# Kernel optimization log

Hardware: AMD Instinct MI355X
Metric: run time of the kernel (lower is better)

## Reference

```python
import jax, jax.numpy as jnp
import numpy as np

BN_EPS = 1e-5


def _bn(x, gamma, beta):
    # BatchNorm1d in training mode: batch mean, biased variance
    m = jnp.mean(x, axis=0)
    v = jnp.var(x, axis=0)
    return (x - m) * jax.lax.rsqrt(v + BN_EPS) * gamma + beta


def _gin_rel(h_src, h_dst, src, dst, W1, W2, g1, b1, g2, b2):
    # GINConv (eps=0): sum-aggregate src features onto dst, add self feature
    n_dst = h_dst.shape[0]
    agg = jax.ops.segment_sum(h_src[src], dst, num_segments=n_dst)  # [N_dst, d]
    x = h_dst + agg
    # MLP: Linear -> BN -> ReLU -> Linear  (both Linears bias=False)
    h = jax.nn.relu(_bn(x @ W1, g1, b1)) @ W2
    # GINBase: BN -> ReLU
    return jax.nn.relu(_bn(h, g2, b2))


def setup_inputs() -> dict:
    key = jax.random.key(0)
    ks = jax.random.split(key, 12)
    N_U, N_I, E, D = 50000, 50000, 640000, 128
    s = 1.0 / np.sqrt(D)
    inp = {
        "h_user": jax.random.normal(ks[0], (N_U, D), jnp.float32),
        "h_item": jax.random.normal(ks[1], (N_I, D), jnp.float32),
        "src_rates": jax.random.randint(ks[2], (E,), 0, N_U, jnp.int32),
        "dst_rates": jax.random.randint(ks[3], (E,), 0, N_I, jnp.int32),
        "src_rev": jax.random.randint(ks[4], (E,), 0, N_I, jnp.int32),
        "dst_rev": jax.random.randint(ks[5], (E,), 0, N_U, jnp.int32),
        "W1_rates": jax.random.normal(ks[6], (D, D), jnp.float32) * s,
        "W2_rates": jax.random.normal(ks[7], (D, D), jnp.float32) * s,
        "g1_rates": jnp.ones((D,), jnp.float32),
        "b1_rates": jnp.zeros((D,), jnp.float32),
        "g2_rates": jnp.ones((D,), jnp.float32),
        "b2_rates": jnp.zeros((D,), jnp.float32),
        "W1_rev": jax.random.normal(ks[8], (D, D), jnp.float32) * s,
        "W2_rev": jax.random.normal(ks[9], (D, D), jnp.float32) * s,
        "g1_rev": jnp.ones((D,), jnp.float32),
        "b1_rev": jnp.zeros((D,), jnp.float32),
        "g2_rev": jnp.ones((D,), jnp.float32),
        "b2_rev": jnp.zeros((D,), jnp.float32),
    }
    return inp


def reference(h_user, h_item, src_rates, dst_rates, src_rev, dst_rev,
              W1_rates, W2_rates, g1_rates, b1_rates, g2_rates, b2_rates,
              W1_rev, W2_rev, g1_rev, b1_rev, g2_rev, b2_rev):
    # relation 'rates': user -> item; relation 'rated_by': item -> user
    out_item = _gin_rel(h_user, h_item, src_rates, dst_rates,
                        W1_rates, W2_rates, g1_rates, b1_rates, g2_rates, b2_rates)
    out_user = _gin_rel(h_item, h_user, src_rev, dst_rev,
                        W1_rev, W2_rev, g1_rev, b1_rev, g2_rev, b2_rev)
    # HeteroGraphConv sums per dst type; one relation per dst type here.
    # GINLayer squeezes each output (no-op for 2D tensors).
    return (out_user, out_item)
```

## Files before the change

### kernel.cpp

```cpp
#include <hip/hip_runtime.h>

#define D 128
static constexpr float BN_EPS = 1e-5f;

typedef __attribute__((ext_vector_type(8))) short short8;
typedef __attribute__((ext_vector_type(4))) float f32x4;

__device__ __forceinline__ unsigned short f2bf(float f)
{
    unsigned u = __builtin_bit_cast(unsigned, f);
    unsigned r = u + 0x7fffu + ((u >> 16) & 1u);
    return (unsigned short)(r >> 16);
}
__device__ __forceinline__ float bflo(unsigned u)
{
    return __builtin_bit_cast(float, u << 16);
}
__device__ __forceinline__ float bfhi(unsigned u)
{
    return __builtin_bit_cast(float, u & 0xffff0000u);
}

struct CsrRel {
    const int* src; const int* dst;
    int* counts; int* offsets; int* bsum; int* perm; int* rank;
    int E; int N; int nscan;
};
struct GatherRel {
    const unsigned short* hb; const float* hdst;
    const int* offsets; const int* perm;
    unsigned short* x; int N;
};
struct GemmRel {
    const unsigned short* X; const unsigned short* Wt;
    const float* insum; const float* insq; const float* gg; const float* bb;
    unsigned short* Y; float* osum; float* osq;
    int N; int ntiles;
};
struct OutRel {
    const unsigned short* z;
    const float* sum; const float* sq; const float* gg; const float* bb;
    float* out; int N;
};

__global__ void convert_h_kernel(const float* __restrict__ hu,
                                 const float* __restrict__ hi,
                                 unsigned short* __restrict__ bu,
                                 unsigned short* __restrict__ bi8,
                                 int nu8, int ni8)
{
    int i = blockIdx.x * blockDim.x + threadIdx.x;
    if (i >= nu8 + ni8) return;
    const float* s; unsigned short* d; int o;
    if (i < nu8) { s = hu; d = bu; o = i; }
    else         { s = hi; d = bi8; o = i - nu8; }
    float4 v0 = reinterpret_cast<const float4*>(s)[o * 2];
    float4 v1 = reinterpret_cast<const float4*>(s)[o * 2 + 1];
    uint4 r;
    r.x = (unsigned)f2bf(v0.x) | ((unsigned)f2bf(v0.y) << 16);
    r.y = (unsigned)f2bf(v0.z) | ((unsigned)f2bf(v0.w) << 16);
    r.z = (unsigned)f2bf(v1.x) | ((unsigned)f2bf(v1.y) << 16);
    r.w = (unsigned)f2bf(v1.z) | ((unsigned)f2bf(v1.w) << 16);
    reinterpret_cast<uint4*>(d)[o] = r;
}

__global__ __launch_bounds__(256) void prep_w_kernel(
    const float* __restrict__ Wa, const float* __restrict__ Wb,
    const float* __restrict__ Wc, const float* __restrict__ Wd,
    unsigned short* __restrict__ wt)
{
    const int wsel = blockIdx.x >> 4;
    const float* W = wsel == 0 ? Wa : wsel == 1 ? Wb : wsel == 2 ? Wc : Wd;
    unsigned short* out = wt + (size_t)wsel * D * D;
    const int tile = blockIdx.x & 15;
    const int k0 = (tile >> 2) * 32, n0 = (tile & 3) * 32;
    __shared__ float s[32][33];
    const int t = threadIdx.x;
    const int r = t >> 3, c = (t & 7) * 4;
    float4 v = *reinterpret_cast<const float4*>(W + (size_t)(k0 + r) * D + n0 + c);
    s[r][c] = v.x; s[r][c + 1] = v.y; s[r][c + 2] = v.z; s[r][c + 3] = v.w;
    __syncthreads();
    unsigned lo = (unsigned)f2bf(s[c][r]) | ((unsigned)f2bf(s[c + 1][r]) << 16);
    unsigned hi = (unsigned)f2bf(s[c + 2][r]) | ((unsigned)f2bf(s[c + 3][r]) << 16);
    *reinterpret_cast<uint2*>(out + (size_t)(n0 + r) * D + k0 + c) =
        make_uint2(lo, hi);
}

__global__ void hist_kernel(CsrRel r0, CsrRel r1)
{
    CsrRel r = blockIdx.y ? r1 : r0;
    int e = blockIdx.x * blockDim.x + threadIdx.x;
    if (e < r.E) r.rank[e] = atomicAdd(&r.counts[r.dst[e]], 1);
}

__global__ __launch_bounds__(256) void scan_partial_kernel(CsrRel rr0, CsrRel rr1)
{
    CsrRel r = blockIdx.y ? rr1 : rr0;
    if ((int)blockIdx.x >= r.nscan) return;
    __shared__ int red[256];
    const int t = threadIdx.x;
    const int base = blockIdx.x * 1024 + t * 4;
    int s = 0;
    if (base + 3 < r.N) {
        int4 q = *reinterpret_cast<const int4*>(r.counts + base);
        s = q.x + q.y + q.z + q.w;
    } else {
        for (int j = 0; j < 4; ++j)
            if (base + j < r.N) s += r.counts[base + j];
    }
    red[t] = s;
    __syncthreads();
    for (int off = 128; off > 0; off >>= 1) {
        if (t < off) red[t] += red[t + off];
        __syncthreads();
    }
    if (t == 0) r.bsum[blockIdx.x] = red[0];
}

__global__ __launch_bounds__(256) void scan_partials_kernel(CsrRel rr0, CsrRel rr1)
{
    CsrRel r = blockIdx.y ? rr1 : rr0;
    __shared__ int part[256];
    const int t = threadIdx.x;
    int v = (t < r.nscan) ? r.bsum[t] : 0;
    part[t] = v;
    __syncthreads();
    for (int off = 1; off < 256; off <<= 1) {
        int tmp = (t >= off) ? part[t - off] : 0;
        __syncthreads();
        part[t] += tmp;
        __syncthreads();
    }
    if (t < r.nscan) r.bsum[t] = part[t] - v;
}

__global__ __launch_bounds__(256) void scan_block_kernel(CsrRel rr0, CsrRel rr1)
{
    CsrRel r = blockIdx.y ? rr1 : rr0;
    if ((int)blockIdx.x >= r.nscan) return;
    __shared__ int part[256];
    const int b = blockIdx.x, t = threadIdx.x;
    const int base = b * 1024 + t * 4;
    int v[4] = {0, 0, 0, 0};
    if (base + 3 < r.N) {
        int4 q = *reinterpret_cast<const int4*>(r.counts + base);
        v[0] = q.x; v[1] = q.y; v[2] = q.z; v[3] = q.w;
    } else {
        for (int j = 0; j < 4; ++j)
            if (base + j < r.N) v[j] = r.counts[base + j];
    }
    int s = v[0] + v[1] + v[2] + v[3];
    part[t] = s;
    __syncthreads();
    for (int off = 1; off < 256; off <<= 1) {
        int tmp = (t >= off) ? part[t - off] : 0;
        __syncthreads();
        part[t] += tmp;
        __syncthreads();
    }
    int excl = part[t] - s + r.bsum[b];
    int o0 = excl, o1 = o0 + v[0], o2 = o1 + v[1], o3 = o2 + v[2];
    if (base + 3 < r.N) {
        *reinterpret_cast<int4*>(r.offsets + base) = make_int4(o0, o1, o2, o3);
    } else {
        int oo[4] = {o0, o1, o2, o3};
        for (int j = 0; j < 4; ++j)
            if (base + j < r.N) r.offsets[base + j] = oo[j];
    }
    if (b == r.nscan - 1 && t == 255) r.offsets[r.N] = r.bsum[b] + part[255];
}

#define FILL_EPT 8
__global__ __launch_bounds__(256) void fill_kernel(CsrRel rr0, CsrRel rr1)
{
    CsrRel r = blockIdx.y ? rr1 : rr0;
    const int bucket = blockIdx.x & 7;
    const int chunk = blockIdx.x >> 3;
    const int nper = (r.N + 7) >> 3;
    const int lo = bucket * nper, hi = lo + nper;
    const int base = chunk * (256 * FILL_EPT) + threadIdx.x;
#pragma unroll
    for (int k = 0; k < FILL_EPT; ++k) {
        int e = base + k * 256;
        if (e < r.E) {
            int d = r.dst[e];
            if (d >= lo && d < hi)
                r.perm[r.offsets[d] + r.rank[e]] = r.src[e];
        }
    }
}

__global__ __launch_bounds__(256) void gather_agg_kernel(GatherRel g0, GatherRel g1)
{
    GatherRel g = blockIdx.y ? g1 : g0;
    int row = blockIdx.x * 4 + (threadIdx.x >> 6);
    row = __builtin_amdgcn_readfirstlane(row);
    if (row >= g.N) return;
    const int c = (threadIdx.x & 63) * 2;
    const int beg = g.offsets[row], end = g.offsets[row + 1];
    float2 acc = *reinterpret_cast<const float2*>(g.hdst + (size_t)row * D + c);
    const unsigned short* hb = g.hb;
    int i = beg;
    for (; i + 3 < end; i += 4) {
        int s0 = g.perm[i], s1 = g.perm[i + 1];
        int s2 = g.perm[i + 2], s3 = g.perm[i + 3];
        unsigned u0 = *reinterpret_cast<const unsigned*>(hb + (size_t)s0 * D + c);
        unsigned u1 = *reinterpret_cast<const unsigned*>(hb + (size_t)s1 * D + c);
        unsigned u2 = *reinterpret_cast<const unsigned*>(hb + (size_t)s2 * D + c);
        unsigned u3 = *reinterpret_cast<const unsigned*>(hb + (size_t)s3 * D + c);
        acc.x += (bflo(u0) + bflo(u1)) + (bflo(u2) + bflo(u3));
        acc.y += (bfhi(u0) + bfhi(u1)) + (bfhi(u2) + bfhi(u3));
    }
    for (; i < end; ++i) {
        unsigned u = *reinterpret_cast<const unsigned*>(hb + (size_t)g.perm[i] * D + c);
        acc.x += bflo(u);
        acc.y += bfhi(u);
    }
    unsigned o = (unsigned)f2bf(acc.x) | ((unsigned)f2bf(acc.y) << 16);
    *reinterpret_cast<unsigned*>(g.x + (size_t)row * D + c) = o;
}

__device__ __forceinline__ unsigned bnpack(unsigned u, float sLo, float sHi,
                                           float bLo, float bHi)
{
    float lo = fmaxf(fmaf(bflo(u), sLo, bLo), 0.f);
    float hi = fmaxf(fmaf(bfhi(u), sHi, bHi), 0.f);
    return (unsigned)f2bf(lo) | ((unsigned)f2bf(hi) << 16);
}

template <bool BN_IN>
__global__ __launch_bounds__(256, 2) void gemm_stats_kernel(GemmRel q0, GemmRel q1)
{
    GemmRel q = blockIdx.y ? q1 : q0;
    const int t = threadIdx.x;
    const int w = t >> 6;
    const int l = t & 63;
    const int lr = l & 15;
    const int lk = (l >> 4) << 3;

    __shared__ float s_sc[D], s_bi[D];
    if constexpr (BN_IN) {
        if (t < D) {
            float inv_n = 1.f / (float)q.N;
            float mean = q.insum[t] * inv_n;
            float var = fmaxf(q.insq[t] * inv_n - mean * mean, 0.f);
            float s = q.gg[t] * rsqrtf(var + BN_EPS);
            s_sc[t] = s;
            s_bi[t] = q.bb[t] - mean * s;
        }
        __syncthreads();
    }

    uint4 wf[4][8];
#pragma unroll
    for (int kk = 0; kk < 4; ++kk)
#pragma unroll
        for (int n = 0; n < 8; ++n)
            wf[kk][n] = *reinterpret_cast<const uint4*>(
                q.Wt + (size_t)(n * 16 + lr) * D + kk * 32 + lk);

    float ps[8], pq[8];
#pragma unroll
    for (int n = 0; n < 8; ++n) { ps[n] = 0.f; pq[n] = 0.f; }

    for (int tile = blockIdx.x; tile < q.ntiles; tile += gridDim.x) {
        const int arow = tile * 64 + w * 16 + lr;
        f32x4 acc[8];
#pragma unroll
        for (int n = 0; n < 8; ++n) acc[n] = (f32x4){0.f, 0.f, 0.f, 0.f};

#pragma unroll
        for (int kk = 0; kk < 4; ++kk) {
            uint4 a4 = make_uint4(0u, 0u, 0u, 0u);
            if (arow < q.N) {
                a4 = *reinterpret_cast<const uint4*>(
                    q.X + (size_t)arow * D + kk * 32 + lk);
                if constexpr (BN_IN) {
                    const int kb = kk * 32 + lk;
                    float4 s0 = *reinterpret_cast<const float4*>(&s_sc[kb]);
                    float4 s1 = *reinterpret_cast<const float4*>(&s_sc[kb + 4]);
                    float4 b0 = *reinterpret_cast<const float4*>(&s_bi[kb]);
                    float4 b1 = *reinterpret_cast<const float4*>(&s_bi[kb + 4]);
                    a4.x = bnpack(a4.x, s0.x, s0.y, b0.x, b0.y);
                    a4.y = bnpack(a4.y, s0.z, s0.w, b0.z, b0.w);
                    a4.z = bnpack(a4.z, s1.x, s1.y, b1.x, b1.y);
                    a4.w = bnpack(a4.w, s1.z, s1.w, b1.z, b1.w);
                }
            }
            short8 a = __builtin_bit_cast(short8, a4);
#pragma unroll
            for (int n = 0; n < 8; ++n)
                acc[n] = __builtin_amdgcn_mfma_f32_16x16x32_bf16(
                    a, __builtin_bit_cast(short8, wf[kk][n]), acc[n], 0, 0, 0);
        }

        const int orow = tile * 64 + w * 16 + (l >> 4) * 4;
#pragma unroll
        for (int n = 0; n < 8; ++n) {
#pragma unroll
            for (int j = 0; j < 4; ++j) {
                float v = acc[n][j];
                ps[n] += v;
                pq[n] += v * v;
                if (orow + j < q.N)
                    q.Y[(size_t)(orow + j) * D + n * 16 + lr] = f2bf(v);
            }
        }
    }

#pragma unroll
    for (int n = 0; n < 8; ++n) {
        ps[n] += __shfl_xor(ps[n], 16); ps[n] += __shfl_xor(ps[n], 32);
        pq[n] += __shfl_xor(pq[n], 16); pq[n] += __shfl_xor(pq[n], 32);
    }
    __shared__ float ssum[4][D], ssq[4][D];
    if (l < 16) {
#pragma unroll
        for (int n = 0; n < 8; ++n) {
            ssum[w][n * 16 + l] = ps[n];
            ssq[w][n * 16 + l]  = pq[n];
        }
    }
    __syncthreads();
    if (t < D) {
        float a = ssum[0][t] + ssum[1][t] + ssum[2][t] + ssum[3][t];
        float b = ssq[0][t] + ssq[1][t] + ssq[2][t] + ssq[3][t];
        atomicAdd(&q.osum[t], a);
        atomicAdd(&q.osq[t], b);
    }
}

__global__ __launch_bounds__(256) void bn_relu_out_kernel(OutRel o0, OutRel o1)
{
    OutRel o = blockIdx.y ? o1 : o0;
    __shared__ float s_sc[D], s_bi[D];
    if (threadIdx.x < D) {
        int c = threadIdx.x;
        float inv_n = 1.f / (float)o.N;
        float mean = o.sum[c] * inv_n;
        float var = fmaxf(o.sq[c] * inv_n - mean * mean, 0.f);
        float s = o.gg[c] * rsqrtf(var + BN_EPS);
        s_sc[c] = s;
        s_bi[c] = o.bb[c] - mean * s;
    }
    __syncthreads();

    const int n8 = o.N * (D / 8);
    for (int i = blockIdx.x * blockDim.x + threadIdx.x; i < n8;
         i += gridDim.x * blockDim.x) {
        uint4 z = reinterpret_cast<const uint4*>(o.z)[i];
        int c = (i * 8) & (D - 1);
        float4 s0 = *reinterpret_cast<const float4*>(&s_sc[c]);
        float4 s1 = *reinterpret_cast<const float4*>(&s_sc[c + 4]);
        float4 b0 = *reinterpret_cast<const float4*>(&s_bi[c]);
        float4 b1 = *reinterpret_cast<const float4*>(&s_bi[c + 4]);
        float4 r0, r1;
        r0.x = fmaxf(fmaf(bflo(z.x), s0.x, b0.x), 0.f);
        r0.y = fmaxf(fmaf(bfhi(z.x), s0.y, b0.y), 0.f);
        r0.z = fmaxf(fmaf(bflo(z.y), s0.z, b0.z), 0.f);
        r0.w = fmaxf(fmaf(bfhi(z.y), s0.w, b0.w), 0.f);
        r1.x = fmaxf(fmaf(bflo(z.z), s1.x, b1.x), 0.f);
        r1.y = fmaxf(fmaf(bfhi(z.z), s1.y, b1.y), 0.f);
        r1.z = fmaxf(fmaf(bflo(z.w), s1.z, b1.z), 0.f);
        r1.w = fmaxf(fmaf(bfhi(z.w), s1.w, b1.w), 0.f);
        reinterpret_cast<float4*>(o.out)[i * 2] = r0;
        reinterpret_cast<float4*>(o.out)[i * 2 + 1] = r1;
    }
}

extern "C" void kernel_launch(void* const* d_in, const int* in_sizes, int n_in,
                              void* d_out, int out_size, void* d_ws, size_t ws_size,
                              hipStream_t stream)
{
    const float* h_user   = (const float*)d_in[0];
    const float* h_item   = (const float*)d_in[1];
    const int* src_rates  = (const int*)d_in[2];
    const int* dst_rates  = (const int*)d_in[3];
    const int* src_rev    = (const int*)d_in[4];
    const int* dst_rev    = (const int*)d_in[5];
    const float* W1_rates = (const float*)d_in[6];
    const float* W2_rates = (const float*)d_in[7];
    const float* g1_rates = (const float*)d_in[8];
    const float* b1_rates = (const float*)d_in[9];
    const float* g2_rates = (const float*)d_in[10];
    const float* b2_rates = (const float*)d_in[11];
    const float* W1_rev   = (const float*)d_in[12];
    const float* W2_rev   = (const float*)d_in[13];
    const float* g1_rev   = (const float*)d_in[14];
    const float* b1_rev   = (const float*)d_in[15];
    const float* g2_rev   = (const float*)d_in[16];
    const float* b2_rev   = (const float*)d_in[17];

    const int n_user = in_sizes[0] / D;
    const int n_item = in_sizes[1] / D;
    const int E1 = in_sizes[2];
    const int E2 = in_sizes[4];

    char* p = (char*)d_ws;
    auto alloc = [&](size_t bytes) {
        char* q = p;
        p += (bytes + 255) & ~(size_t)255;
        return q;
    };
    unsigned short* hbu = (unsigned short*)alloc((size_t)n_user * D * 2);
    unsigned short* hbi = (unsigned short*)alloc((size_t)n_item * D * 2);
    unsigned short* xz0 = (unsigned short*)alloc((size_t)n_item * D * 2);
    unsigned short* xz1 = (unsigned short*)alloc((size_t)n_user * D * 2);
    unsigned short* yb0 = (unsigned short*)alloc((size_t)n_item * D * 2);
    unsigned short* yb1 = (unsigned short*)alloc((size_t)n_user * D * 2);
    unsigned short* wt  = (unsigned short*)alloc((size_t)4 * D * D * 2);
    char* zbeg = p;
    float* stats   = (float*)alloc((size_t)8 * D * 4);
    int* counts0   = (int*)alloc((size_t)n_item * 4);
    int* counts1   = (int*)alloc((size_t)n_user * 4);
    size_t zbytes  = (size_t)(p - zbeg);
    int* offsets0  = (int*)alloc(((size_t)n_item + 1) * 4);
    int* offsets1  = (int*)alloc(((size_t)n_user + 1) * 4);
    int* bsum0     = (int*)alloc((size_t)256 * 4);
    int* bsum1     = (int*)alloc((size_t)256 * 4);
    int* perm0     = (int*)alloc((size_t)E1 * 4);
    int* perm1     = (int*)alloc((size_t)E2 * 4);
    int* rank0     = (int*)alloc((size_t)E1 * 4);
    int* rank1     = (int*)alloc((size_t)E2 * 4);

    float* out_user = (float*)d_out;
    float* out_item = out_user + (size_t)n_user * D;

    const int nu8 = n_user * D / 8, ni8 = n_item * D / 8;
    convert_h_kernel<<<(nu8 + ni8 + 255) / 256, 256, 0, stream>>>(
        h_user, h_item, hbu, hbi, nu8, ni8);
    prep_w_kernel<<<64, 256, 0, stream>>>(W1_rates, W2_rates, W1_rev, W2_rev, wt);
    hipMemsetAsync(zbeg, 0, zbytes, stream);

    float* st0 = stats;
    float* st1 = stats + 4 * D;

    CsrRel c0 = {src_rates, dst_rates, counts0, offsets0, bsum0, perm0, rank0,
                 E1, n_item, (n_item + 1023) / 1024};
    CsrRel c1 = {src_rev, dst_rev, counts1, offsets1, bsum1, perm1, rank1,
                 E2, n_user, (n_user + 1023) / 1024};

    int emax = E1 > E2 ? E1 : E2;
    int eb = (emax + 255) / 256;
    int ns = c0.nscan > c1.nscan ? c0.nscan : c1.nscan;
    hist_kernel<<<dim3(eb, 2), 256, 0, stream>>>(c0, c1);
    scan_partial_kernel<<<dim3(ns, 2), 256, 0, stream>>>(c0, c1);
    scan_partials_kernel<<<dim3(1, 2), 256, 0, stream>>>(c0, c1);
    scan_block_kernel<<<dim3(ns, 2), 256, 0, stream>>>(c0, c1);
    int fb = 8 * ((emax + 256 * FILL_EPT - 1) / (256 * FILL_EPT));
    fill_kernel<<<dim3(fb, 2), 256, 0, stream>>>(c0, c1);

    GatherRel ga0 = {hbu, h_item, offsets0, perm0, xz0, n_item};
    GatherRel ga1 = {hbi, h_user, offsets1, perm1, xz1, n_user};
    int ab = ((n_item > n_user ? n_item : n_user) + 3) / 4;
    gather_agg_kernel<<<dim3(ab, 2), 256, 0, stream>>>(ga0, ga1);

    const int nt0 = (n_item + 63) / 64, nt1 = (n_user + 63) / 64;
    int gx = nt0 > nt1 ? nt0 : nt1;
    if (gx > 256) gx = 256;

    GemmRel q10 = {xz0, wt,             nullptr, nullptr, nullptr, nullptr,
                   yb0, st0, st0 + D, n_item, nt0};
    GemmRel q11 = {xz1, wt + 2 * D * D, nullptr, nullptr, nullptr, nullptr,
                   yb1, st1, st1 + D, n_user, nt1};
    gemm_stats_kernel<false><<<dim3(gx, 2), 256, 0, stream>>>(q10, q11);

    GemmRel q20 = {yb0, wt + D * D,     st0, st0 + D, g1_rates, b1_rates,
                   xz0, st0 + 2 * D, st0 + 3 * D, n_item, nt0};
    GemmRel q21 = {yb1, wt + 3 * D * D, st1, st1 + D, g1_rev, b1_rev,
                   xz1, st1 + 2 * D, st1 + 3 * D, n_user, nt1};
    gemm_stats_kernel<true><<<dim3(gx, 2), 256, 0, stream>>>(q20, q21);

    OutRel o0 = {xz0, st0 + 2 * D, st0 + 3 * D, g2_rates, b2_rates,
                 out_item, n_item};
    OutRel o1 = {xz1, st1 + 2 * D, st1 + 3 * D, g2_rev, b2_rev,
                 out_user, n_user};
    int n8m = (n_item > n_user ? n_item : n_user) * (D / 8);
    int ob = (n8m + 255) / 256;
    if (ob > 2048) ob = 2048;
    bn_relu_out_kernel<<<dim3(ob, 2), 256, 0, stream>>>(o0, o1);
}
```

Before: 223.7 us.

## Build CSR histogram with LDS-privatized per-bucket-chunk counters instead of global atomics

Replaces global atomic histogramming with blocks that each own a destination bucket and edge chunk and count into shared memory. A new per-destination prefix pass over chunks produces the per-chunk offsets and the total counts, and the fill kernel adds the chunk offset to the local rank. This removes contended global atomics and the memset of the counts array. In exchange it adds a kernel launch and a partial-count buffer, and each block rescans its whole edge chunk, so every edge is read once per bucket. The 8192-entry shared array must hold a full bucket width, which caps N at about 65k.

```diff
diff --git a/kernel.cpp b/kernel.cpp
--- a/kernel.cpp
+++ b/kernel.cpp
@@ -1,6 +1,9 @@
 #include <hip/hip_runtime.h>
 
 #define D 128
+#define NBUK 8
+#define NCH 32
+#define BWMAX 8192
 static constexpr float BN_EPS = 1e-5f;
 
 typedef __attribute__((ext_vector_type(8))) short short8;
@@ -23,7 +26,7 @@
 
 struct CsrRel {
     const int* src; const int* dst;
-    int* counts; int* offsets; int* bsum; int* perm; int* rank;
+    int* counts; int* offsets; int* bsum; int* perm; int* rank; int* pc;
     int E; int N; int nscan;
 };
 struct GatherRel {
@@ -86,11 +89,45 @@
         make_uint2(lo, hi);
 }
 
-__global__ void hist_kernel(CsrRel r0, CsrRel r1)
+__global__ __launch_bounds__(256) void hist_kernel(CsrRel r0, CsrRel r1)
 {
     CsrRel r = blockIdx.y ? r1 : r0;
-    int e = blockIdx.x * blockDim.x + threadIdx.x;
-    if (e < r.E) r.rank[e] = atomicAdd(&r.counts[r.dst[e]], 1);
+    __shared__ int h[BWMAX];
+    const int b = blockIdx.x & (NBUK - 1);
+    const int c = blockIdx.x >> 3;
+    const int bw = (r.N + NBUK - 1) / NBUK;
+    const int lo = b * bw;
+    const int hi = min(lo + bw, r.N);
+    const int CE = (r.E + NCH - 1) / NCH;
+    const int e1 = min(c * CE + CE, r.E);
+
+    for (int j = threadIdx.x; j < bw; j += 256) h[j] = 0;
+    __syncthreads();
+    for (int e = c * CE + threadIdx.x; e < e1; e += 256) {
+        int d = r.dst[e];
+        if (d >= lo && d < hi)
+            r.rank[e] = atomicAdd(&h[d - lo], 1);
+    }
+    __syncthreads();
+    int* out = r.pc + (size_t)(b * NCH + c) * bw;
+    for (int j = threadIdx.x; j < bw; j += 256) out[j] = h[j];
+}
+
+__global__ __launch_bounds__(256) void chunkpfx_kernel(CsrRel r0, CsrRel r1)
+{
+    CsrRel r = blockIdx.y ? r1 : r0;
+    int d = blockIdx.x * 256 + threadIdx.x;
+    if (d >= r.N) return;
+    const int bw = (r.N + NBUK - 1) / NBUK;
+    int b = d / bw, j = d - b * bw;
+    int* base = r.pc + (size_t)b * NCH * bw + j;
+    int s = 0;
+    for (int c = 0; c < NCH; ++c) {
+        int t = base[(size_t)c * bw];
+        base[(size_t)c * bw] = s;
+        s += t;
+    }
+    r.counts[d] = s;
 }
 
 __global__ __launch_bounds__(256) void scan_partial_kernel(CsrRel rr0, CsrRel rr1)
@@ -170,23 +207,21 @@
     if (b == r.nscan - 1 && t == 255) r.offsets[r.N] = r.bsum[b] + part[255];
 }
 
-#define FILL_EPT 8
 __global__ __launch_bounds__(256) void fill_kernel(CsrRel rr0, CsrRel rr1)
 {
     CsrRel r = blockIdx.y ? rr1 : rr0;
-    const int bucket = blockIdx.x & 7;
-    const int chunk = blockIdx.x >> 3;
-    const int nper = (r.N + 7) >> 3;
-    const int lo = bucket * nper, hi = lo + nper;
-    const int base = chunk * (256 * FILL_EPT) + threadIdx.x;
-#pragma unroll
-    for (int k = 0; k < FILL_EPT; ++k) {
-        int e = base + k * 256;
-        if (e < r.E) {
-            int d = r.dst[e];
-            if (d >= lo && d < hi)
-                r.perm[r.offsets[d] + r.rank[e]] = r.src[e];
-        }
+    const int b = blockIdx.x & (NBUK - 1);
+    const int c = blockIdx.x >> 3;
+    const int bw = (r.N + NBUK - 1) / NBUK;
+    const int lo = b * bw;
+    const int hi = min(lo + bw, r.N);
+    const int CE = (r.E + NCH - 1) / NCH;
+    const int e1 = min(c * CE + CE, r.E);
+    const int* pcb = r.pc + (size_t)(b * NCH + c) * bw;
+    for (int e = c * CE + threadIdx.x; e < e1; e += 256) {
+        int d = r.dst[e];
+        if (d >= lo && d < hi)
+            r.perm[r.offsets[d] + pcb[d - lo] + r.rank[e]] = r.src[e];
     }
 }
 
@@ -396,6 +431,9 @@
     const int E1 = in_sizes[2];
     const int E2 = in_sizes[4];
 
+    const int bw0 = (n_item + NBUK - 1) / NBUK;
+    const int bw1 = (n_user + NBUK - 1) / NBUK;
+
     char* p = (char*)d_ws;
     auto alloc = [&](size_t bytes) {
         char* q = p;
@@ -409,11 +447,9 @@
     unsigned short* yb0 = (unsigned short*)alloc((size_t)n_item * D * 2);
     unsigned short* yb1 = (unsigned short*)alloc((size_t)n_user * D * 2);
     unsigned short* wt  = (unsigned short*)alloc((size_t)4 * D * D * 2);
-    char* zbeg = p;
     float* stats   = (float*)alloc((size_t)8 * D * 4);
     int* counts0   = (int*)alloc((size_t)n_item * 4);
     int* counts1   = (int*)alloc((size_t)n_user * 4);
-    size_t zbytes  = (size_t)(p - zbeg);
     int* offsets0  = (int*)alloc(((size_t)n_item + 1) * 4);
     int* offsets1  = (int*)alloc(((size_t)n_user + 1) * 4);
     int* bsum0     = (int*)alloc((size_t)256 * 4);
@@ -422,6 +458,8 @@
     int* perm1     = (int*)alloc((size_t)E2 * 4);
     int* rank0     = (int*)alloc((size_t)E1 * 4);
     int* rank1     = (int*)alloc((size_t)E2 * 4);
+    int* pc0       = (int*)alloc((size_t)NBUK * NCH * bw0 * 4);
+    int* pc1       = (int*)alloc((size_t)NBUK * NCH * bw1 * 4);
 
     float* out_user = (float*)d_out;
     float* out_item = out_user + (size_t)n_user * D;
@@ -430,29 +468,28 @@
     convert_h_kernel<<<(nu8 + ni8 + 255) / 256, 256, 0, stream>>>(
         h_user, h_item, hbu, hbi, nu8, ni8);
     prep_w_kernel<<<64, 256, 0, stream>>>(W1_rates, W2_rates, W1_rev, W2_rev, wt);
-    hipMemsetAsync(zbeg, 0, zbytes, stream);
+    hipMemsetAsync(stats, 0, 8 * D * sizeof(float), stream);
 
     float* st0 = stats;
     float* st1 = stats + 4 * D;
 
     CsrRel c0 = {src_rates, dst_rates, counts0, offsets0, bsum0, perm0, rank0,
-                 E1, n_item, (n_item + 1023) / 1024};
+                 pc0, E1, n_item, (n_item + 1023) / 1024};
     CsrRel c1 = {src_rev, dst_rev, counts1, offsets1, bsum1, perm1, rank1,
-                 E2, n_user, (n_user + 1023) / 1024};
-
-    int emax = E1 > E2 ? E1 : E2;
-    int eb = (emax + 255) / 256;
+                 pc1, E2, n_user, (n_user + 1023) / 1024};
+
     int ns = c0.nscan > c1.nscan ? c0.nscan : c1.nscan;
-    hist_kernel<<<dim3(eb, 2), 256, 0, stream>>>(c0, c1);
+    int nmax = n_item > n_user ? n_item : n_user;
+    hist_kernel<<<dim3(NBUK * NCH, 2), 256, 0, stream>>>(c0, c1);
+    chunkpfx_kernel<<<dim3((nmax + 255) / 256, 2), 256, 0, stream>>>(c0, c1);
     scan_partial_kernel<<<dim3(ns, 2), 256, 0, stream>>>(c0, c1);
     scan_partials_kernel<<<dim3(1, 2), 256, 0, stream>>>(c0, c1);
     scan_block_kernel<<<dim3(ns, 2), 256, 0, stream>>>(c0, c1);
-    int fb = 8 * ((emax + 256 * FILL_EPT - 1) / (256 * FILL_EPT));
-    fill_kernel<<<dim3(fb, 2), 256, 0, stream>>>(c0, c1);
+    fill_kernel<<<dim3(NBUK * NCH, 2), 256, 0, stream>>>(c0, c1);
 
     GatherRel ga0 = {hbu, h_item, offsets0, perm0, xz0, n_item};
     GatherRel ga1 = {hbi, h_user, offsets1, perm1, xz1, n_user};
-    int ab = ((n_item > n_user ? n_item : n_user) + 3) / 4;
+    int ab = (nmax + 3) / 4;
     gather_agg_kernel<<<dim3(ab, 2), 256, 0, stream>>>(ga0, ga1);
 
     const int nt0 = (n_item + 63) / 64, nt1 = (n_user + 63) / 64;
@@ -475,7 +512,7 @@
                  out_item, n_item};
     OutRel o1 = {xz1, st1 + 2 * D, st1 + 3 * D, g2_rev, b2_rev,
                  out_user, n_user};
-    int n8m = (n_item > n_user ? n_item : n_user) * (D / 8);
+    int n8m = nmax * (D / 8);
     int ob = (n8m + 255) / 256;
     if (ob > 2048) ob = 2048;
     bn_relu_out_kernel<<<dim3(ob, 2), 256, 0, stream>>>(o0, o1);
```

Result: slower. 242.4 us (+8.4%).
